# Performance work log

Measured on AMD Instinct MI355X. Metric: run time of the kernel, lower is better.

Reference implementation:

```python
import jax, jax.numpy as jnp
import numpy as np

N_NODES = 50000
N_NEIB = 64
D = 256
BATCH = 1024
N_SAMPLES = (25, 10)  # fanout per layer (layer_specs n_sample)


def setup_inputs() -> dict:
    key = jax.random.key(0)
    ks = jax.random.split(key, 12)
    inp = {
        'ids': jax.random.randint(ks[0], (BATCH,), 0, N_NODES),
        'diff_idx': jax.random.randint(ks[1], (N_NODES, N_NEIB), 0, N_NODES),
        'diff_val': jax.random.uniform(ks[2], (N_NODES, N_NEIB), dtype=jnp.float32),
        'feats': jax.random.normal(ks[3], (N_NODES, D), dtype=jnp.float32),
    }
    # two aggregator layers, each: fc_x, fc_neib : D -> D (= output_dim//2)
    for li in range(2):
        inp[f'Wx{li+1}'] = jax.random.normal(ks[4 + 4 * li], (D, D), dtype=jnp.float32) * 0.05
        inp[f'bx{li+1}'] = jnp.zeros((D,), dtype=jnp.float32)
        inp[f'Wn{li+1}'] = jax.random.normal(ks[5 + 4 * li], (D, D), dtype=jnp.float32) * 0.05
        inp[f'bn{li+1}'] = jnp.zeros((D,), dtype=jnp.float32)
    return inp


def _sample(diff_idx, diff_val, ids, n_samples, key):
    # gather candidate neighbor rows, shared random column permutation, take first n_samples
    tmp_idx = diff_idx[ids]            # [n, N_NEIB]
    tmp_val = diff_val[ids]
    perm = jax.random.permutation(key, tmp_idx.shape[1])
    idx = tmp_idx[:, perm][:, :n_samples].reshape(-1)
    val = tmp_val[:, perm][:, :n_samples].reshape(-1)
    return idx, val


def _agg(x, neib, vals, Wx, bx, Wn, bn):
    # weighted-mean neighbor aggregation + self/neib linear combine + relu
    n = x.shape[0]
    d = neib.shape[1]
    neib = neib.reshape(n, -1, d)              # [n, s, d]
    vals = vals.reshape(n, -1)                 # [n, s]
    w = vals / (jnp.sum(vals, axis=1, keepdims=True) + 1e-10)
    m = jnp.einsum('nsd,ns->nd', neib, w)      # weighted mean of neighbors
    return jax.nn.relu(x @ Wx + bx + m @ Wn + bn)


def reference(ids, diff_idx, diff_val, feats,
              Wx1, bx1, Wn1, bn1, Wx2, bx2, Wn2, bn2):
    skey = jax.random.key(42)
    all_feats = [feats[ids]]
    all_vals = []
    cur = ids
    for li, n in enumerate(N_SAMPLES):
        cur, vals = _sample(diff_idx, diff_val, cur, n, jax.random.fold_in(skey, li))
        all_feats.append(feats[cur])
        all_vals.append(vals)
    params = [(Wx1, bx1, Wn1, bn1), (Wx2, bx2, Wn2, bn2)]
    for Wx, bx, Wn, bn in params:
        all_feats = [_agg(all_feats[k], all_feats[k + 1], all_vals[k], Wx, bx, Wn, bn)
                     for k in range(len(all_feats) - 1)]
    assert len(all_feats) == 1
    return all_feats[0]  # [BATCH, D]
```

## Files before the change

kernel.cpp:

```cpp
#include <hip/hip_runtime.h>
#include <stdint.h>
#include <stddef.h>
#include <algorithm>

#define BATCH  1024
#define S1     25
#define S2     10
#define DIM    256
#define NNEIB  64
#define L2ROWS (BATCH * S1)
#define MROWS  (BATCH + BATCH * S1)
#define KTOT   512
#define NFEAT  50000

struct Perm25 { int p[S1]; };
struct Perm10 { int p[S2]; };

typedef __attribute__((ext_vector_type(8))) short short8;
typedef __attribute__((ext_vector_type(4))) float f32x4;

static inline uint32_t rotl_(uint32_t x, int d) { return (x << d) | (x >> (32 - d)); }

static void tf2x32(uint32_t k0, uint32_t k1, uint32_t x0, uint32_t x1,
                   uint32_t* o0, uint32_t* o1) {
  const uint32_t ks0 = k0, ks1 = k1, ks2 = k0 ^ k1 ^ 0x1BD11BDAu;
  static const int R[8] = {13, 15, 26, 6, 17, 29, 16, 24};
  x0 += ks0; x1 += ks1;
  for (int g = 0; g < 5; ++g) {
    const int* rr = R + (g & 1) * 4;
    for (int i = 0; i < 4; i++) { x0 += x1; x1 = rotl_(x1, rr[i]); x1 ^= x0; }
    uint32_t a, b;
    switch (g) {
      default:
      case 0: a = ks1; b = ks2; break;
      case 1: a = ks2; b = ks0; break;
      case 2: a = ks0; b = ks1; break;
      case 3: a = ks1; b = ks2; break;
      case 4: a = ks2; b = ks0; break;
    }
    x0 += a; x1 = x1 + b + (uint32_t)(g + 1);
  }
  *o0 = x0; *o1 = x1;
}

static void compute_perm(uint32_t li, int n, int* out) {
  uint32_t k0, k1, s0, s1;
  tf2x32(0u, 42u, 0u, li, &k0, &k1);
  tf2x32(k0, k1, 0u, 1u, &s0, &s1);
  uint32_t bits[NNEIB];
  for (int i = 0; i < NNEIB; i++) {
    uint32_t a, b;
    tf2x32(s0, s1, 0u, (uint32_t)i, &a, &b);
    bits[i] = a ^ b;
  }
  int idx[NNEIB];
  for (int i = 0; i < NNEIB; i++) idx[i] = i;
  std::stable_sort(idx, idx + NNEIB, [&](int A, int B) { return bits[A] < bits[B]; });
  for (int j = 0; j < n; j++) out[j] = idx[j];
}

__device__ __forceinline__ unsigned short f2bf(float x) {
  union { float f; uint32_t u; } v; v.f = x;
  uint32_t r = (v.u + 0x7FFFu + ((v.u >> 16) & 1u)) >> 16;
  return (unsigned short)r;
}
__device__ __forceinline__ float bfbits2f(uint32_t lo16) {
  union { uint32_t u; float f; } v; v.u = lo16 << 16;
  return v.f;
}


#define PREP_CONVF   12500
#define PREP_CONVW   512
#define PREP_BLOCKS  (PREP_CONVF + 2 * PREP_CONVW + 4)
__global__ __launch_bounds__(256) void prep_k(
    const float* __restrict__ feats, uint32_t* __restrict__ fb,
    const float* __restrict__ Wx1, const float* __restrict__ Wn1,
    unsigned short* __restrict__ Wt1,
    const float* __restrict__ Wx2, const float* __restrict__ Wn2,
    unsigned short* __restrict__ Wt2,
    const int* __restrict__ ids, const int* __restrict__ dix,
    const float* __restrict__ dval, int* __restrict__ idx1,
    float* __restrict__ w1, Perm25 pm) {
  int b = blockIdx.x, t = threadIdx.x;
  if (b < PREP_CONVF) {
    int i = b * 256 + t;
    f32x4 v = *(const f32x4*)&feats[(size_t)i * 4];
    fb[(size_t)i * 2]     = f2bf(v.x) | ((uint32_t)f2bf(v.y) << 16);
    fb[(size_t)i * 2 + 1] = f2bf(v.z) | ((uint32_t)f2bf(v.w) << 16);
  } else if (b < PREP_CONVF + 2 * PREP_CONVW) {
    int wi = b - PREP_CONVF;
    const float* Wx = (wi < PREP_CONVW) ? Wx1 : Wx2;
    const float* Wn = (wi < PREP_CONVW) ? Wn1 : Wn2;
    unsigned short* Wt = (wi < PREP_CONVW) ? Wt1 : Wt2;
    int idx = (wi % PREP_CONVW) * 256 + t;
    int n = idx >> 9, k = idx & 511;
    float v = (k < DIM) ? Wx[(size_t)k * DIM + n] : Wn[(size_t)(k - DIM) * DIM + n];
    Wt[(size_t)n * KTOT + k] = f2bf(v);
  } else {
    int i = (b - PREP_CONVF - 2 * PREP_CONVW) * 256 + t;
    if (i >= BATCH) return;
    int nid = ids[i];
    const float* vr = dval + (size_t)nid * NNEIB;
    const int* ir = dix + (size_t)nid * NNEIB;
    float v[S1];
    float s = 0.f;
    for (int j = 0; j < S1; j++) { v[j] = vr[pm.p[j]]; s += v[j]; }
    float inv = 1.f / (s + 1e-10f);
    for (int j = 0; j < S1; j++) {
      w1[i * S1 + j] = v[j] * inv;
      idx1[i * S1 + j] = ir[pm.p[j]];
    }
  }
}

__global__ __launch_bounds__(256) void stage1_k(
    const uint2* __restrict__ fb, const int* __restrict__ idx1,
    const float* __restrict__ w1, const int* __restrict__ dix,
    const float* __restrict__ dval, Perm10 pm2, uint2* __restrict__ M1) {
  int wave = threadIdx.x >> 6, lane = threadIdx.x & 63;
  int r = blockIdx.x * 4 + wave;
  int s, nbl = 0;
  float wl = 0.f;
  if (r < BATCH) {
    s = S1;
    if (lane < S1) { nbl = idx1[r * S1 + lane]; wl = w1[r * S1 + lane]; }
  } else {
    s = S2;
    int nx = idx1[r - BATCH];
    float vj = 0.f;
    if (lane < S2) {
      int c = pm2.p[lane];
      nbl = dix[(size_t)nx * NNEIB + c];
      vj = dval[(size_t)nx * NNEIB + c];
    }
    float tot = 0.f;
    for (int j = 0; j < S2; j++) tot += __shfl(vj, j);
    wl = vj / (tot + 1e-10f);
  }
  float a0 = 0.f, a1 = 0.f, a2 = 0.f, a3 = 0.f;
  for (int j = 0; j < s; j++) {
    int nid = __shfl(nbl, j);
    float wj = __shfl(wl, j);
    uint2 u = fb[(size_t)nid * 64 + lane];
    a0 += wj * bfbits2f(u.x & 0xffffu);
    a1 += wj * bfbits2f(u.x >> 16);
    a2 += wj * bfbits2f(u.y & 0xffffu);
    a3 += wj * bfbits2f(u.y >> 16);
  }
  uint2 o;
  o.x = f2bf(a0) | ((uint32_t)f2bf(a1) << 16);
  o.y = f2bf(a2) | ((uint32_t)f2bf(a3) << 16);
  M1[(size_t)r * 64 + lane] = o;
}

__global__ __launch_bounds__(256) void stage2_k(
    const uint2* __restrict__ Hb, const float* __restrict__ w1,
    uint2* __restrict__ M2) {
  int wave = threadIdx.x >> 6, lane = threadIdx.x & 63;
  int i = blockIdx.x * 4 + wave;
  float wl = (lane < S1) ? w1[(size_t)i * S1 + lane] : 0.f;
  const uint2* hb = Hb + (size_t)(BATCH + i * S1) * 64 + lane;
  float a0 = 0.f, a1 = 0.f, a2 = 0.f, a3 = 0.f;
  for (int j = 0; j < S1; j++) {
    float wj = __shfl(wl, j);
    uint2 u = hb[(size_t)j * 64];
    a0 += wj * bfbits2f(u.x & 0xffffu);
    a1 += wj * bfbits2f(u.x >> 16);
    a2 += wj * bfbits2f(u.y & 0xffffu);
    a3 += wj * bfbits2f(u.y >> 16);
  }
  uint2 o;
  o.x = f2bf(a0) | ((uint32_t)f2bf(a1) << 16);
  o.y = f2bf(a2) | ((uint32_t)f2bf(a3) << 16);
  M2[(size_t)i * 64 + lane] = o;
}

#define BK 32
#define LPAD 40
template <int TBM, int TBN, bool OUT_BF16>
__global__ __launch_bounds__(256) void gemm_k(
    const unsigned short* __restrict__ Xsrc, const int* __restrict__ ids,
    const int* __restrict__ idx1, const unsigned short* __restrict__ Mh,
    const unsigned short* __restrict__ Wt, const float* __restrict__ bx,
    const float* __restrict__ bn, void* __restrict__ OutP) {
  constexpr int MI = TBM / 32;
  constexpr int NJ = TBN / 32;
  __shared__ __align__(16) unsigned short As[TBM][LPAD];
  __shared__ __align__(16) unsigned short Bs[TBN][LPAD];
  int t = threadIdx.x;
  int wave = t >> 6, lane = t & 63, quad = lane >> 4, l16 = lane & 15;
  int wm = (wave >> 1) * (TBM / 2);
  int wn = (wave & 1) * (TBN / 2);
  int row0 = blockIdx.x * TBM, col0 = blockIdx.y * TBN;

  f32x4 acc[MI][NJ];
#pragma unroll
  for (int i = 0; i < MI; i++)
#pragma unroll
    for (int j = 0; j < NJ; j++) acc[i][j] = (f32x4){0.f, 0.f, 0.f, 0.f};

  int lr = t >> 2;
  int lq = (t & 3) * 8;
  int xrow[TBM / 64];
#pragma unroll
  for (int p = 0; p < TBM / 64; p++) {
    int gr = row0 + p * 64 + lr;
    xrow[p] = ids ? ((gr < BATCH) ? ids[gr] : idx1[gr - BATCH]) : gr;
  }

  for (int k0 = 0; k0 < KTOT; k0 += BK) {
#pragma unroll
    for (int p = 0; p < TBM / 64; p++) {
      const unsigned short* src =
          (k0 < DIM) ? (Xsrc + (size_t)xrow[p] * DIM + k0 + lq)
                     : (Mh + (size_t)(row0 + p * 64 + lr) * DIM + (k0 - DIM) + lq);
      *(f32x4*)&As[p * 64 + lr][lq] = *(const f32x4*)src;
    }
#pragma unroll
    for (int p = 0; p < TBN / 64; p++)
      *(f32x4*)&Bs[p * 64 + lr][lq] =
          *(const f32x4*)&Wt[(size_t)(col0 + p * 64 + lr) * KTOT + k0 + lq];
    __syncthreads();

    short8 af[MI], bfr[NJ];
#pragma unroll
    for (int i = 0; i < MI; i++)
      af[i] = *(const short8*)&As[wm + i * 16 + l16][quad * 8];
#pragma unroll
    for (int j = 0; j < NJ; j++)
      bfr[j] = *(const short8*)&Bs[wn + j * 16 + l16][quad * 8];
#pragma unroll
    for (int i = 0; i < MI; i++)
#pragma unroll
      for (int j = 0; j < NJ; j++)
        acc[i][j] = __builtin_amdgcn_mfma_f32_16x16x32_bf16(af[i], bfr[j], acc[i][j], 0, 0, 0);
    __syncthreads();
  }

  float bias[NJ];
#pragma unroll
  for (int j = 0; j < NJ; j++) {
    int c = col0 + wn + j * 16 + l16;
    bias[j] = bx[c] + bn[c];
  }
#pragma unroll
  for (int i = 0; i < MI; i++) {
#pragma unroll
    for (int j = 0; j < NJ; j++) {
      int c = col0 + wn + j * 16 + l16;
#pragma unroll
      for (int reg = 0; reg < 4; reg++) {
        int r = row0 + wm + i * 16 + quad * 4 + reg;
        float v = fmaxf(acc[i][j][reg] + bias[j], 0.f);
        if (OUT_BF16)
          ((unsigned short*)OutP)[(size_t)r * DIM + c] = f2bf(v);
        else
          ((float*)OutP)[(size_t)r * DIM + c] = v;
      }
    }
  }
}

static inline size_t align256(size_t x) { return (x + 255) & ~(size_t)255; }

extern "C" void kernel_launch(void* const* d_in, const int* in_sizes, int n_in,
                              void* d_out, int out_size, void* d_ws, size_t ws_size,
                              hipStream_t stream) {
  const int*   ids  = (const int*)d_in[0];
  const int*   dix  = (const int*)d_in[1];
  const float* dval = (const float*)d_in[2];
  const float* feats= (const float*)d_in[3];
  const float* Wx1  = (const float*)d_in[4];
  const float* bx1  = (const float*)d_in[5];
  const float* Wn1  = (const float*)d_in[6];
  const float* bn1  = (const float*)d_in[7];
  const float* Wx2  = (const float*)d_in[8];
  const float* bx2  = (const float*)d_in[9];
  const float* Wn2  = (const float*)d_in[10];
  const float* bn2  = (const float*)d_in[11];
  float* out = (float*)d_out;

  Perm25 p25;
  Perm10 p10;
  compute_perm(0u, S1, p25.p);
  compute_perm(1u, S2, p10.p);

  char* w = (char*)d_ws;
  int*            idx1 = (int*)w;            w += align256(sizeof(int) * L2ROWS);
  float*          w1   = (float*)w;          w += align256(sizeof(float) * L2ROWS);
  uint32_t*       fb   = (uint32_t*)w;       w += align256(2 * (size_t)NFEAT * DIM);
  unsigned short* M1   = (unsigned short*)w; w += align256(2 * (size_t)MROWS * DIM);
  unsigned short* Hb   = (unsigned short*)w; w += align256(2 * (size_t)MROWS * DIM);
  unsigned short* M2   = (unsigned short*)w; w += align256(2 * (size_t)BATCH * DIM);
  unsigned short* Wt1  = (unsigned short*)w; w += align256(2 * (size_t)DIM * KTOT);
  unsigned short* Wt2  = (unsigned short*)w; w += align256(2 * (size_t)DIM * KTOT);

  prep_k<<<PREP_BLOCKS, 256, 0, stream>>>(feats, fb, Wx1, Wn1, Wt1, Wx2, Wn2, Wt2,
                                          ids, dix, dval, idx1, w1, p25);
  stage1_k<<<MROWS / 4, 256, 0, stream>>>((const uint2*)fb, idx1, w1, dix, dval, p10,
                                          (uint2*)M1);
  gemm_k<128, 128, true><<<dim3(MROWS / 128, DIM / 128), 256, 0, stream>>>(
      (const unsigned short*)fb, ids, idx1, M1, Wt1, bx1, bn1, Hb);
  stage2_k<<<BATCH / 4, 256, 0, stream>>>((const uint2*)Hb, w1, (uint2*)M2);
  gemm_k<64, 64, false><<<dim3(BATCH / 64, DIM / 64), 256, 0, stream>>>(
      Hb, nullptr, nullptr, M2, Wt2, bx2, bn2, out);
}
```

Baseline: 188.1 us.

## Fuse layer-2 aggregation into final GEMM and deepen K tile of layer-1 GEMM

Removes the separate stage2 aggregation kernel. The layer-2 weighted neighbour mean is now computed per block into shared memory and fed straight into a new fused GEMM kernel, which drops one launch and the M2 global round-trip. The layer-1 GEMM also gets a templated K tile (64 instead of 32), halving its loop iterations and syncs. The fused kernel recomputes the aggregation once per column tile (two column tiles), duplicating that gather work, and runs with only 64 small blocks.

After: 193.4 us. 2.8% more time.

```diff
diff --git a/kernel.cpp b/kernel.cpp
--- a/kernel.cpp
+++ b/kernel.cpp
@@ -154,44 +154,22 @@
   M1[(size_t)r * 64 + lane] = o;
 }
 
-__global__ __launch_bounds__(256) void stage2_k(
-    const uint2* __restrict__ Hb, const float* __restrict__ w1,
-    uint2* __restrict__ M2) {
-  int wave = threadIdx.x >> 6, lane = threadIdx.x & 63;
-  int i = blockIdx.x * 4 + wave;
-  float wl = (lane < S1) ? w1[(size_t)i * S1 + lane] : 0.f;
-  const uint2* hb = Hb + (size_t)(BATCH + i * S1) * 64 + lane;
-  float a0 = 0.f, a1 = 0.f, a2 = 0.f, a3 = 0.f;
-  for (int j = 0; j < S1; j++) {
-    float wj = __shfl(wl, j);
-    uint2 u = hb[(size_t)j * 64];
-    a0 += wj * bfbits2f(u.x & 0xffffu);
-    a1 += wj * bfbits2f(u.x >> 16);
-    a2 += wj * bfbits2f(u.y & 0xffffu);
-    a3 += wj * bfbits2f(u.y >> 16);
-  }
-  uint2 o;
-  o.x = f2bf(a0) | ((uint32_t)f2bf(a1) << 16);
-  o.y = f2bf(a2) | ((uint32_t)f2bf(a3) << 16);
-  M2[(size_t)i * 64 + lane] = o;
-}
-
-#define BK 32
-#define LPAD 40
-template <int TBM, int TBN, bool OUT_BF16>
+template <int TBM, int TBN, int TBK, bool OUT_BF16>
 __global__ __launch_bounds__(256) void gemm_k(
     const unsigned short* __restrict__ Xsrc, const int* __restrict__ ids,
     const int* __restrict__ idx1, const unsigned short* __restrict__ Mh,
     const unsigned short* __restrict__ Wt, const float* __restrict__ bx,
     const float* __restrict__ bn, void* __restrict__ OutP) {
-  constexpr int MI = TBM / 32;
-  constexpr int NJ = TBN / 32;
-  __shared__ __align__(16) unsigned short As[TBM][LPAD];
-  __shared__ __align__(16) unsigned short Bs[TBN][LPAD];
+  constexpr int MI = TBM / 32, NJ = TBN / 32;
+  constexpr int KP = TBK + 8;
+  constexpr int CPR = TBK / 8;
+  constexpr int APASS = TBM * TBK / 2048;
+  constexpr int BPASS = TBN * TBK / 2048;
+  __shared__ __align__(16) unsigned short As[TBM][KP];
+  __shared__ __align__(16) unsigned short Bs[TBN][KP];
   int t = threadIdx.x;
   int wave = t >> 6, lane = t & 63, quad = lane >> 4, l16 = lane & 15;
-  int wm = (wave >> 1) * (TBM / 2);
-  int wn = (wave & 1) * (TBN / 2);
+  int wm = (wave >> 1) * (TBM / 2), wn = (wave & 1) * (TBN / 2);
   int row0 = blockIdx.x * TBM, col0 = blockIdx.y * TBN;
 
   f32x4 acc[MI][NJ];
@@ -200,41 +178,47 @@
 #pragma unroll
     for (int j = 0; j < NJ; j++) acc[i][j] = (f32x4){0.f, 0.f, 0.f, 0.f};
 
-  int lr = t >> 2;
-  int lq = (t & 3) * 8;
-  int xrow[TBM / 64];
-#pragma unroll
-  for (int p = 0; p < TBM / 64; p++) {
-    int gr = row0 + p * 64 + lr;
+  int arow[APASS], akc[APASS], xrow[APASS];
+#pragma unroll
+  for (int p = 0; p < APASS; p++) {
+    int cid = p * 256 + t;
+    arow[p] = cid / CPR;
+    akc[p] = (cid % CPR) * 8;
+    int gr = row0 + arow[p];
     xrow[p] = ids ? ((gr < BATCH) ? ids[gr] : idx1[gr - BATCH]) : gr;
   }
 
-  for (int k0 = 0; k0 < KTOT; k0 += BK) {
-#pragma unroll
-    for (int p = 0; p < TBM / 64; p++) {
+  for (int k0 = 0; k0 < KTOT; k0 += TBK) {
+#pragma unroll
+    for (int p = 0; p < APASS; p++) {
       const unsigned short* src =
-          (k0 < DIM) ? (Xsrc + (size_t)xrow[p] * DIM + k0 + lq)
-                     : (Mh + (size_t)(row0 + p * 64 + lr) * DIM + (k0 - DIM) + lq);
-      *(f32x4*)&As[p * 64 + lr][lq] = *(const f32x4*)src;
-    }
-#pragma unroll
-    for (int p = 0; p < TBN / 64; p++)
-      *(f32x4*)&Bs[p * 64 + lr][lq] =
-          *(const f32x4*)&Wt[(size_t)(col0 + p * 64 + lr) * KTOT + k0 + lq];
+          (k0 < DIM) ? (Xsrc + (size_t)xrow[p] * DIM + k0 + akc[p])
+                     : (Mh + (size_t)(row0 + arow[p]) * DIM + (k0 - DIM) + akc[p]);
+      *(f32x4*)&As[arow[p]][akc[p]] = *(const f32x4*)src;
+    }
+#pragma unroll
+    for (int p = 0; p < BPASS; p++) {
+      int cid = p * 256 + t;
+      int br = cid / CPR, bkc = (cid % CPR) * 8;
+      *(f32x4*)&Bs[br][bkc] =
+          *(const f32x4*)&Wt[(size_t)(col0 + br) * KTOT + k0 + bkc];
+    }
     __syncthreads();
-
-    short8 af[MI], bfr[NJ];
-#pragma unroll
-    for (int i = 0; i < MI; i++)
-      af[i] = *(const short8*)&As[wm + i * 16 + l16][quad * 8];
-#pragma unroll
-    for (int j = 0; j < NJ; j++)
-      bfr[j] = *(const short8*)&Bs[wn + j * 16 + l16][quad * 8];
-#pragma unroll
-    for (int i = 0; i < MI; i++)
+#pragma unroll
+    for (int kk = 0; kk < TBK; kk += 32) {
+      short8 af[MI], bfr[NJ];
+#pragma unroll
+      for (int i = 0; i < MI; i++)
+        af[i] = *(const short8*)&As[wm + i * 16 + l16][kk + quad * 8];
 #pragma unroll
       for (int j = 0; j < NJ; j++)
-        acc[i][j] = __builtin_amdgcn_mfma_f32_16x16x32_bf16(af[i], bfr[j], acc[i][j], 0, 0, 0);
+        bfr[j] = *(const short8*)&Bs[wn + j * 16 + l16][kk + quad * 8];
+#pragma unroll
+      for (int i = 0; i < MI; i++)
+#pragma unroll
+        for (int j = 0; j < NJ; j++)
+          acc[i][j] = __builtin_amdgcn_mfma_f32_16x16x32_bf16(af[i], bfr[j], acc[i][j], 0, 0, 0);
+    }
     __syncthreads();
   }
 
@@ -258,6 +242,82 @@
         else
           ((float*)OutP)[(size_t)r * DIM + c] = v;
       }
+    }
+  }
+}
+
+#define MS_PAD 264
+#define LPAD2 40
+__global__ __launch_bounds__(256) void gemm2f_k(
+    const unsigned short* __restrict__ Hb, const float* __restrict__ w1,
+    const unsigned short* __restrict__ Wt, const float* __restrict__ bx,
+    const float* __restrict__ bn, float* __restrict__ out) {
+  __shared__ __align__(16) unsigned short Ms[32][MS_PAD];
+  __shared__ __align__(16) unsigned short As[32][LPAD2];
+  __shared__ __align__(16) unsigned short Bs[128][LPAD2];
+  int t = threadIdx.x;
+  int wave = t >> 6, lane = t & 63, quad = lane >> 4, l16 = lane & 15;
+  int row0 = blockIdx.x * 32, col0 = blockIdx.y * 128;
+  int wm = (wave >> 1) * 16, wn = (wave & 1) * 64;
+
+  const uint2* Hb2 = (const uint2*)Hb;
+#pragma unroll
+  for (int rr = 0; rr < 8; rr++) {
+    int m = wave * 8 + rr;
+    int i = row0 + m;
+    float wl = (lane < S1) ? w1[(size_t)i * S1 + lane] : 0.f;
+    const uint2* hb = Hb2 + (size_t)(BATCH + i * S1) * 64 + lane;
+    float a0 = 0.f, a1 = 0.f, a2 = 0.f, a3 = 0.f;
+    for (int j = 0; j < S1; j++) {
+      float wj = __shfl(wl, j);
+      uint2 u = hb[(size_t)j * 64];
+      a0 += wj * bfbits2f(u.x & 0xffffu);
+      a1 += wj * bfbits2f(u.x >> 16);
+      a2 += wj * bfbits2f(u.y & 0xffffu);
+      a3 += wj * bfbits2f(u.y >> 16);
+    }
+    uint2 o;
+    o.x = f2bf(a0) | ((uint32_t)f2bf(a1) << 16);
+    o.y = f2bf(a2) | ((uint32_t)f2bf(a3) << 16);
+    *(uint2*)&Ms[m][lane * 4] = o;
+  }
+
+  f32x4 acc[4];
+#pragma unroll
+  for (int j = 0; j < 4; j++) acc[j] = (f32x4){0.f, 0.f, 0.f, 0.f};
+
+  for (int k0 = 0; k0 < KTOT; k0 += 32) {
+    if (k0 < DIM) {
+      if (t < 128) {
+        int br = t >> 2, kc = (t & 3) * 8;
+        *(f32x4*)&As[br][kc] = *(const f32x4*)&Hb[(size_t)(row0 + br) * DIM + k0 + kc];
+      }
+    }
+#pragma unroll
+    for (int p = 0; p < 2; p++) {
+      int cid = p * 256 + t;
+      int br = cid >> 2, kc = (cid & 3) * 8;
+      *(f32x4*)&Bs[br][kc] = *(const f32x4*)&Wt[(size_t)(col0 + br) * KTOT + k0 + kc];
+    }
+    __syncthreads();
+    short8 af = (k0 < DIM) ? *(const short8*)&As[wm + l16][quad * 8]
+                           : *(const short8*)&Ms[wm + l16][(k0 - DIM) + quad * 8];
+#pragma unroll
+    for (int j = 0; j < 4; j++) {
+      short8 bf = *(const short8*)&Bs[wn + j * 16 + l16][quad * 8];
+      acc[j] = __builtin_amdgcn_mfma_f32_16x16x32_bf16(af, bf, acc[j], 0, 0, 0);
+    }
+    __syncthreads();
+  }
+
+#pragma unroll
+  for (int j = 0; j < 4; j++) {
+    int c = col0 + wn + j * 16 + l16;
+    float bias = bx[c] + bn[c];
+#pragma unroll
+    for (int reg = 0; reg < 4; reg++) {
+      int r = row0 + wm + quad * 4 + reg;
+      out[(size_t)r * DIM + c] = fmaxf(acc[j][reg] + bias, 0.f);
     }
   }
 }
@@ -292,7 +352,6 @@
   uint32_t*       fb   = (uint32_t*)w;       w += align256(2 * (size_t)NFEAT * DIM);
   unsigned short* M1   = (unsigned short*)w; w += align256(2 * (size_t)MROWS * DIM);
   unsigned short* Hb   = (unsigned short*)w; w += align256(2 * (size_t)MROWS * DIM);
-  unsigned short* M2   = (unsigned short*)w; w += align256(2 * (size_t)BATCH * DIM);
   unsigned short* Wt1  = (unsigned short*)w; w += align256(2 * (size_t)DIM * KTOT);
   unsigned short* Wt2  = (unsigned short*)w; w += align256(2 * (size_t)DIM * KTOT);
 
@@ -300,9 +359,8 @@
                                           ids, dix, dval, idx1, w1, p25);
   stage1_k<<<MROWS / 4, 256, 0, stream>>>((const uint2*)fb, idx1, w1, dix, dval, p10,
                                           (uint2*)M1);
-  gemm_k<128, 128, true><<<dim3(MROWS / 128, DIM / 128), 256, 0, stream>>>(
+  gemm_k<128, 128, 64, true><<<dim3(MROWS / 128, DIM / 128), 256, 0, stream>>>(
       (const unsigned short*)fb, ids, idx1, M1, Wt1, bx1, bn1, Hb);
-  stage2_k<<<BATCH / 4, 256, 0, stream>>>((const uint2*)Hb, w1, (uint2*)M2);
-  gemm_k<64, 64, false><<<dim3(BATCH / 64, DIM / 64), 256, 0, stream>>>(
-      Hb, nullptr, nullptr, M2, Wt2, bx2, bn2, out);
-}
+  gemm2f_k<<<dim3(BATCH / 32, DIM / 128), 256, 0, stream>>>(
+      Hb, w1, Wt2, bx2, bn2, out);
+}
```
